# Performance work log

Measured on AMD Instinct MI355X. Metric: run time of the kernel, lower is better.

The kernel has to match this reference:

```python
import jax, jax.numpy as jnp
import numpy as np

D = 4096
N = 8192


def fwht(x):
    """Fast Walsh-Hadamard Transform (orthonormal, divided by sqrt(d)).

    log2(d) butterfly stages, each a single vectorized add/sub over the
    full tensor. Loop bound is static (log2 of trailing dim), jit-safe.
    """
    d = x.shape[-1]
    leading = x.shape[:-1]
    h = 1
    while h < d:
        x = x.reshape(*leading, d // (2 * h), 2, h)
        a = x[..., 0, :]
        b = x[..., 1, :]
        x = jnp.stack([a + b, a - b], axis=-2).reshape(*leading, d)
        h *= 2
    return x * jnp.asarray(d, x.dtype) ** -0.5


def setup_inputs() -> dict:
    key = jax.random.key(0)
    kx, ks = jax.random.split(key)
    x = jax.random.normal(kx, (N, D), dtype=jnp.float32)
    # deterministic random +/-1 sign vector (buffer of RHTRotation)
    signs = (jax.random.randint(ks, (D,), 0, 2).astype(jnp.float32) * 2.0 - 1.0)
    return {"x": x, "signs": signs}


def reference(x, signs):
    # randomized_hadamard: y = H @ (D x) / sqrt(d), D = diag(signs)
    return fwht(x * signs)
```

## Files before the change

### kernel.cpp

```cpp
#include <hip/hip_runtime.h>

#define D 4096

__device__ __forceinline__ void fwht64(float v[64]) {
#pragma unroll
    for (int s = 1; s < 64; s <<= 1) {
#pragma unroll
        for (int i = 0; i < 64; i++) {
            if (!(i & s)) {
                float a = v[i], b = v[i ^ s];
                v[i]     = a + b;
                v[i ^ s] = a - b;
            }
        }
    }
}

__global__ __launch_bounds__(64) void fwht_kernel(const float* __restrict__ x,
                                                  const float* __restrict__ signs,
                                                  float* __restrict__ out) {
    __shared__ float lds[4096];

    const int l = threadIdx.x;
    const long row = blockIdx.x;

    float v[64];

    {
        const float4* __restrict__ xv = (const float4*)(x + row * (long)D + l * 64);
        const float4* __restrict__ sv = (const float4*)(signs + l * 64);
#pragma unroll
        for (int k = 0; k < 16; k++) {
            float4 a = xv[k];
            float4 s = sv[k];
            v[4 * k + 0] = a.x * s.x;
            v[4 * k + 1] = a.y * s.y;
            v[4 * k + 2] = a.z * s.z;
            v[4 * k + 3] = a.w * s.w;
        }
    }
    fwht64(v);

#pragma unroll
    for (int r = 0; r < 64; r++) lds[64 * r + (l ^ r)] = v[r];
    asm volatile("s_waitcnt lgkmcnt(0)" ::: "memory");
    __builtin_amdgcn_sched_barrier(0);
#pragma unroll
    for (int r = 0; r < 64; r++) v[r] = lds[64 * l + (l ^ r)];

    fwht64(v);

    const float scale = 1.0f / 64.0f;
    float* __restrict__ orow = out + row * (long)D + l;
#pragma unroll
    for (int r = 0; r < 64; r++) orow[64 * r] = v[r] * scale;
}

extern "C" void kernel_launch(void* const* d_in, const int* in_sizes, int n_in,
                              void* d_out, int out_size, void* d_ws, size_t ws_size,
                              hipStream_t stream) {
    const float* x = (const float*)d_in[0];
    const float* signs = (const float*)d_in[1];
    float* out = (float*)d_out;
    const int rows = in_sizes[0] / D;
    fwht_kernel<<<dim3(rows), dim3(64), 0, stream>>>(x, signs, out);
}
```

Baseline: 245.1 us.

## Process four rows per block with signs cached and next-row prefetch

Each 64-thread block now handles four rows instead of one. The sign vector is loaded once into registers and reused, and the next row's input is loaded while the current row is being transformed, to hide global load latency. The LDS transpose switches to float4 writes with an XOR swizzle. This triples the register arrays, which may cut occupancy, and it quarters the grid size.

Result: slower. 255.1 us (+4.1%).

```diff
diff --git a/kernel.cpp b/kernel.cpp
--- a/kernel.cpp
+++ b/kernel.cpp
@@ -1,6 +1,7 @@
 #include <hip/hip_runtime.h>
 
 #define D 4096
+#define R 4
 
 __device__ __forceinline__ void fwht64(float v[64]) {
 #pragma unroll
@@ -16,44 +17,72 @@
     }
 }
 
-__global__ __launch_bounds__(64) void fwht_kernel(const float* __restrict__ x,
-                                                  const float* __restrict__ signs,
-                                                  float* __restrict__ out) {
+__global__ __launch_bounds__(64, 2) void fwht_kernel(const float* __restrict__ x,
+                                                     const float* __restrict__ signs,
+                                                     float* __restrict__ out) {
     __shared__ float lds[4096];
 
     const int l = threadIdx.x;
-    const long row = blockIdx.x;
+    const long row0 = (long)blockIdx.x * R;
 
-    float v[64];
+    float s[64], u[64], v[64];
 
     {
-        const float4* __restrict__ xv = (const float4*)(x + row * (long)D + l * 64);
         const float4* __restrict__ sv = (const float4*)(signs + l * 64);
 #pragma unroll
         for (int k = 0; k < 16; k++) {
-            float4 a = xv[k];
-            float4 s = sv[k];
-            v[4 * k + 0] = a.x * s.x;
-            v[4 * k + 1] = a.y * s.y;
-            v[4 * k + 2] = a.z * s.z;
-            v[4 * k + 3] = a.w * s.w;
+            float4 g = sv[k];
+            s[4 * k + 0] = g.x; s[4 * k + 1] = g.y;
+            s[4 * k + 2] = g.z; s[4 * k + 3] = g.w;
         }
     }
-    fwht64(v);
+    {
+        const float4* __restrict__ xv = (const float4*)(x + row0 * (long)D + l * 64);
+#pragma unroll
+        for (int k = 0; k < 16; k++) {
+            float4 a = xv[k];
+            u[4 * k + 0] = a.x; u[4 * k + 1] = a.y;
+            u[4 * k + 2] = a.z; u[4 * k + 3] = a.w;
+        }
+    }
 
 #pragma unroll
-    for (int r = 0; r < 64; r++) lds[64 * r + (l ^ r)] = v[r];
-    asm volatile("s_waitcnt lgkmcnt(0)" ::: "memory");
-    __builtin_amdgcn_sched_barrier(0);
+    for (int i = 0; i < R; i++) {
 #pragma unroll
-    for (int r = 0; r < 64; r++) v[r] = lds[64 * l + (l ^ r)];
+        for (int r = 0; r < 64; r++) v[r] = u[r] * s[r];
 
-    fwht64(v);
+        if (i + 1 < R) {
+            const float4* __restrict__ xv =
+                (const float4*)(x + (row0 + i + 1) * (long)D + l * 64);
+#pragma unroll
+            for (int k = 0; k < 16; k++) {
+                float4 a = xv[k];
+                u[4 * k + 0] = a.x; u[4 * k + 1] = a.y;
+                u[4 * k + 2] = a.z; u[4 * k + 3] = a.w;
+            }
+        }
 
-    const float scale = 1.0f / 64.0f;
-    float* __restrict__ orow = out + row * (long)D + l;
+        fwht64(v);
+
 #pragma unroll
-    for (int r = 0; r < 64; r++) orow[64 * r] = v[r] * scale;
+        for (int k = 0; k < 16; k++) {
+            float4 w = make_float4(v[4 * k + 0], v[4 * k + 1],
+                                   v[4 * k + 2], v[4 * k + 3]);
+            *(float4*)&lds[64 * l + 4 * (k ^ (l & 15))] = w;
+        }
+        asm volatile("s_waitcnt lgkmcnt(0)" ::: "memory");
+        __builtin_amdgcn_sched_barrier(0);
+#pragma unroll
+        for (int n = 0; n < 64; n++)
+            v[n] = lds[64 * n + 4 * ((l >> 2) ^ (n & 15)) + (l & 3)];
+
+        fwht64(v);
+
+        const float scale = 1.0f / 64.0f;
+        float* __restrict__ orow = out + (row0 + i) * (long)D + l;
+#pragma unroll
+        for (int n = 0; n < 64; n++) orow[64 * n] = v[n] * scale;
+    }
 }
 
 extern "C" void kernel_launch(void* const* d_in, const int* in_sizes, int n_in,
@@ -63,5 +92,5 @@
     const float* signs = (const float*)d_in[1];
     float* out = (float*)d_out;
     const int rows = in_sizes[0] / D;
-    fwht_kernel<<<dim3(rows), dim3(64), 0, stream>>>(x, signs, out);
+    fwht_kernel<<<dim3(rows / R), dim3(64), 0, stream>>>(x, signs, out);
 }
```
